# Performance work log

Hardware: AMD Instinct MI355X
Metric: run time of the kernel (lower is better)

The kernel has to match this reference:

```python
import jax, jax.numpy as jnp
import numpy as np

H = 64        # hidden_dim
T = 3         # message passing steps
M = 3         # set2set steps
NEF = 4       # num_edge_features
NNF = 11      # num_node_features
NT = 12       # num_targets
N_NODES = 10000
N_EDGES = 50000
B = 256       # number of graphs


def setup_inputs() -> dict:
    key = jax.random.key(0)
    ks = jax.random.split(key, 32)

    def p(k, shape):
        fan_in = shape[-1]
        return jax.random.normal(k, shape, jnp.float32) / np.sqrt(fan_in)

    inp = {}
    inp['x'] = jax.random.normal(ks[0], (N_NODES, NNF), jnp.float32)
    inp['edge_attr'] = jax.random.uniform(ks[1], (N_EDGES, NEF), jnp.float32)
    inp['edge_index'] = jax.random.randint(ks[2], (2, N_EDGES), 0, N_NODES)
    inp['batch'] = jnp.sort(jax.random.randint(ks[3], (N_NODES,), 0, B))
    inp['batch_size'] = B
    # nn1: edge MLP -> per-edge HxH weight
    inp['w1a'] = p(ks[4], (H, NEF)); inp['b1a'] = jnp.zeros((H,), jnp.float32)
    inp['w1b'] = p(ks[5], (H, H));   inp['b1b'] = jnp.zeros((H,), jnp.float32)
    inp['w1c'] = p(ks[6], (H * H, H)); inp['b1c'] = jnp.zeros((H * H,), jnp.float32)
    # GRUCell
    inp['gru_wih'] = p(ks[7], (3 * H, H)); inp['gru_whh'] = p(ks[8], (3 * H, H))
    inp['gru_bih'] = jnp.zeros((3 * H,), jnp.float32); inp['gru_bhh'] = jnp.zeros((3 * H,), jnp.float32)
    # lin: (H + NNF) -> 2H
    inp['lin_w'] = p(ks[9], (2 * H, H + NNF)); inp['lin_b'] = jnp.zeros((2 * H,), jnp.float32)
    # Set2Set 2-layer LSTM: in_channels = 2H, input = 4H, hidden = 2H
    IC = 2 * H
    inp['lstm_wih0'] = p(ks[10], (4 * IC, 2 * IC)); inp['lstm_whh0'] = p(ks[11], (4 * IC, IC))
    inp['lstm_bih0'] = jnp.zeros((4 * IC,), jnp.float32); inp['lstm_bhh0'] = jnp.zeros((4 * IC,), jnp.float32)
    inp['lstm_wih1'] = p(ks[12], (4 * IC, IC)); inp['lstm_whh1'] = p(ks[13], (4 * IC, IC))
    inp['lstm_bih1'] = jnp.zeros((4 * IC,), jnp.float32); inp['lstm_bhh1'] = jnp.zeros((4 * IC,), jnp.float32)
    # nn2: 4H -> 8H -> num_targets
    inp['w2a'] = p(ks[14], (8 * H, 4 * H)); inp['b2a'] = jnp.zeros((8 * H,), jnp.float32)
    inp['w2b'] = p(ks[15], (NT, 8 * H)); inp['b2b'] = jnp.zeros((NT,), jnp.float32)
    return inp


def _gru(x, h, wih, whh, bih, bhh):
    gi = x @ wih.T + bih
    gh = h @ whh.T + bhh
    ir, iz, inn = jnp.split(gi, 3, axis=1)
    hr, hz, hn = jnp.split(gh, 3, axis=1)
    r = jax.nn.sigmoid(ir + hr)
    z = jax.nn.sigmoid(iz + hz)
    n = jnp.tanh(inn + r * hn)
    return (1.0 - z) * n + z * h


def _lstm(x, h, c, wih, whh, bih, bhh):
    g = x @ wih.T + bih + h @ whh.T + bhh
    i, f, gg, o = jnp.split(g, 4, axis=1)
    c_new = jax.nn.sigmoid(f) * c + jax.nn.sigmoid(i) * jnp.tanh(gg)
    h_new = jax.nn.sigmoid(o) * jnp.tanh(c_new)
    return h_new, c_new


def reference(x, edge_attr, w1a, b1a, w1b, b1b, w1c, b1c,
              gru_wih, gru_whh, gru_bih, gru_bhh, lin_w, lin_b,
              lstm_wih0, lstm_whh0, lstm_bih0, lstm_bhh0,
              lstm_wih1, lstm_whh1, lstm_bih1, lstm_bhh1,
              w2a, b2a, w2b, b2b, edge_index, batch, batch_size):
    N = x.shape[0]
    E = edge_attr.shape[0]
    src, dst = edge_index[0], edge_index[1]

    # pad node features into hidden state
    h = jnp.zeros((N, H), x.dtype).at[:, :x.shape[1]].set(x)

    # nn1 edge MLP -> per-edge (H, H) weight (edge_attr constant over T, hoisted)
    e1 = jax.nn.relu(edge_attr @ w1a.T + b1a)
    e1 = jax.nn.relu(e1 @ w1b.T + b1b)
    W_edge = (e1 @ w1c.T + b1c).reshape(E, H, H)  # [E, in, out]

    # T rounds of NNConv (gather -> per-edge matvec -> scatter-add) + GRU
    for _ in range(T):
        m_e = jnp.einsum('eh,eho->eo', h[src], W_edge)
        m = jax.ops.segment_sum(m_e, dst, num_segments=N)
        h = _gru(m, h, gru_wih, gru_whh, gru_bih, gru_bhh)

    h = jnp.concatenate([h, x], axis=1) @ lin_w.T + lin_b  # [N, 2H]

    # Set2Set readout with 2-layer LSTM
    IC = 2 * H
    q_star = jnp.zeros((batch_size, 2 * IC), h.dtype)
    h0 = jnp.zeros((batch_size, IC), h.dtype); c0 = jnp.zeros_like(h0)
    h1 = jnp.zeros_like(h0); c1 = jnp.zeros_like(h0)
    for _ in range(M):
        h0, c0 = _lstm(q_star, h0, c0, lstm_wih0, lstm_whh0, lstm_bih0, lstm_bhh0)
        h1, c1 = _lstm(h0, h1, c1, lstm_wih1, lstm_whh1, lstm_bih1, lstm_bhh1)
        q = h1  # [B, IC]
        e = jnp.sum(h * q[batch], axis=-1)  # [N]
        emax = jax.ops.segment_max(e, batch, num_segments=batch_size)
        a = jnp.exp(e - emax[batch])
        denom = jax.ops.segment_sum(a, batch, num_segments=batch_size)
        a = a / denom[batch]
        r = jax.ops.segment_sum(a[:, None] * h, batch, num_segments=batch_size)
        q_star = jnp.concatenate([q, r], axis=-1)  # [B, 4H]

    out = jax.nn.relu(q_star @ w2a.T + b2a) @ w2b.T + b2b
    return out
```

## Files before the change

### kernel.cpp

```cpp
#include <hip/hip_runtime.h>
#include <math.h>

#define NN 10000
#define NE 50000
#define BG 256
#define NNF 11
#define NT 12

typedef unsigned int u32;
typedef __attribute__((ext_vector_type(8))) short short8v;
typedef __attribute__((ext_vector_type(4))) float f32x4;

__device__ __forceinline__ float sigm(float x){ return 1.0f/(1.0f+__expf(-x)); }
__device__ __forceinline__ u32 f2bf(float f){
  u32 u = __float_as_uint(f);
  return (u + 0x7fffu + ((u>>16)&1u)) >> 16;
}
__device__ __forceinline__ float bf2f(u32 s){ return __uint_as_float(s<<16); }

__global__ __launch_bounds__(256) void k_h_init(const float* __restrict__ x, float* __restrict__ h,
                         unsigned short* __restrict__ hHi, unsigned short* __restrict__ hLo,
                         const float* __restrict__ b1c, float* __restrict__ hb,
                         float* __restrict__ m){
  __shared__ float sv[8][64];
  int t = threadIdx.x, w = t>>6, lane = t&63;
  int n0 = blockIdx.x*8 + w*2;
  #pragma unroll
  for (int q = 0; q < 2; ++q){
    int n = n0 + q;
    float v = (lane < NNF) ? x[n*NNF + lane] : 0.0f;
    h[n*64+lane] = v;
    u32 hv = f2bf(v);
    hHi[n*64+lane] = (unsigned short)hv;
    hLo[n*64+lane] = (unsigned short)f2bf(v - bf2f(hv));
    sv[2*w+q][lane] = v;
  }
  __syncthreads();
  #pragma unroll
  for (int q = 0; q < 2; ++q){
    int n = n0 + q;
    float acc = 0.f;
    #pragma unroll 8
    for (int i = 0; i < 64; ++i) acc = fmaf(sv[2*w+q][i], b1c[i*64+lane], acc);
    hb[n*64+lane] = acc;
    m[n*64+lane] = 0.f;
  }
}

__global__ void k_prep(const float* __restrict__ gwih, const float* __restrict__ gwhh,
                       const float* __restrict__ linw, const float* __restrict__ w1b,
                       const float* __restrict__ wih0, const float* __restrict__ whh0,
                       const float* __restrict__ wih1, const float* __restrict__ whh1,
                       const float* __restrict__ w2a,  const float* __restrict__ w1c,
                       float* __restrict__ wihT, float* __restrict__ whhT,
                       float* __restrict__ linT, unsigned short* __restrict__ w1bB,
                       float* __restrict__ p0i, float* __restrict__ p0h,
                       float* __restrict__ p1i, float* __restrict__ p1h,
                       float* __restrict__ w2aT, unsigned short* __restrict__ qtT,
                       int* __restrict__ deg, float* __restrict__ state0){
  int tid = blockIdx.x*256 + threadIdx.x;
  if (tid < 12288){ int i=tid>>6, j=tid&63; wihT[j*192+i]=gwih[tid]; return; }
  tid -= 12288;
  if (tid < 12288){ int i=tid>>6, j=tid&63; whhT[j*192+i]=gwhh[tid]; return; }
  tid -= 12288;
  if (tid < 9600){ int i=tid/75, j=tid-i*75; linT[j*128+i]=linw[tid]; return; }
  tid -= 9600;
  if (tid < 4096){ w1bB[tid] = (unsigned short)f2bf(w1b[tid]); return; }
  tid -= 4096;
  if (tid < 32768){ int i=tid>>7, j=tid&127;
    float4 v = make_float4(wih0[(j)*256+i], wih0[(128+j)*256+i],
                           wih0[(256+j)*256+i], wih0[(384+j)*256+i]);
    *(float4*)&p0i[tid*4] = v; return; }
  tid -= 32768;
  if (tid < 16384){ int i=tid>>7, j=tid&127;
    float4 v = make_float4(whh0[(j)*128+i], whh0[(128+j)*128+i],
                           whh0[(256+j)*128+i], whh0[(384+j)*128+i]);
    *(float4*)&p0h[tid*4] = v; return; }
  tid -= 16384;
  if (tid < 16384){ int i=tid>>7, j=tid&127;
    float4 v = make_float4(wih1[(j)*128+i], wih1[(128+j)*128+i],
                           wih1[(256+j)*128+i], wih1[(384+j)*128+i]);
    *(float4*)&p1i[tid*4] = v; return; }
  tid -= 16384;
  if (tid < 16384){ int i=tid>>7, j=tid&127;
    float4 v = make_float4(whh1[(j)*128+i], whh1[(128+j)*128+i],
                           whh1[(256+j)*128+i], whh1[(384+j)*128+i]);
    *(float4*)&p1h[tid*4] = v; return; }
  tid -= 16384;
  if (tid < 131072){ int i=tid>>8, j=tid&255; w2aT[j*512+i]=w2a[tid]; return; }
  tid -= 131072;
  if (tid < 262144){ int ko=tid>>6, hh=tid&63; int k=ko>>6, o=ko&63;
                     qtT[tid] = (unsigned short)f2bf(w1c[(hh*64+o)*64+k]); return; }
  tid -= 262144;
  if (tid < NN){ deg[tid] = 0; return; }
  tid -= NN;
  if (tid < 262144) state0[tid] = 0.f;
}

__global__ __launch_bounds__(256) void k_e1m(const float* __restrict__ ea,
                     const float* __restrict__ w1a, const float* __restrict__ b1a,
                     const unsigned short* __restrict__ w1bB, const float* __restrict__ b1b,
                     unsigned short* __restrict__ e1b){
  __shared__ unsigned short sHi[4][16][64], sLo[4][16][64];
  int t = threadIdx.x, w = t>>6, l = t&63;
  int c = l & 15, g = l >> 4;
  int eb = blockIdx.x*64 + w*16;
  float wa0=w1a[l*4+0], wa1=w1a[l*4+1], wa2=w1a[l*4+2], wa3=w1a[l*4+3];
  float bb1 = b1a[l];
  char* hbase = (char*)&sHi[w][0][0];
  char* lbase = (char*)&sLo[w][0][0];
  #pragma unroll
  for (int r = 0; r < 16; ++r){
    int e = eb + r; if (e >= NE) e = NE-1;
    float4 a = *(const float4*)&ea[e*4];
    float h1 = fmaxf(bb1 + a.x*wa0 + a.y*wa1 + a.z*wa2 + a.w*wa3, 0.f);
    u32 hv = f2bf(h1);
    u32 lv = f2bf(h1 - bf2f(hv));
    int wb = (r*128 + l*2) ^ ((r & 7) << 4);
    *(unsigned short*)(hbase + wb) = (unsigned short)hv;
    *(unsigned short*)(lbase + wb) = (unsigned short)lv;
  }
  __syncthreads();
  int xv = (c & 7) << 4;
  int rb0 = (c*128 + g*16) ^ xv;
  int rb1 = (c*128 + 64 + g*16) ^ xv;
  short8v aH0 = *(const short8v*)(hbase + rb0);
  short8v aH1 = *(const short8v*)(hbase + rb1);
  short8v aL0 = *(const short8v*)(lbase + rb0);
  short8v aL1 = *(const short8v*)(lbase + rb1);
  f32x4 acc[4];
  #pragma unroll
  for (int f = 0; f < 4; ++f){
    const short* wrow = (const short*)w1bB + (f*16 + c)*64 + g*8;
    short8v b0 = *(const short8v*)wrow;
    short8v b1 = *(const short8v*)(wrow + 32);
    acc[f] = f32x4{0.f,0.f,0.f,0.f};
    acc[f] = __builtin_amdgcn_mfma_f32_16x16x32_bf16(aH0, b0, acc[f], 0, 0, 0);
    acc[f] = __builtin_amdgcn_mfma_f32_16x16x32_bf16(aL0, b0, acc[f], 0, 0, 0);
    acc[f] = __builtin_amdgcn_mfma_f32_16x16x32_bf16(aH1, b1, acc[f], 0, 0, 0);
    acc[f] = __builtin_amdgcn_mfma_f32_16x16x32_bf16(aL1, b1, acc[f], 0, 0, 0);
  }
  #pragma unroll
  for (int f = 0; f < 4; ++f){
    float bb2 = b1b[f*16 + c];
    #pragma unroll
    for (int r = 0; r < 4; ++r){
      int e = eb + 4*g + r;
      if (e < NE)
        e1b[e*64 + f*16 + c] = (unsigned short)f2bf(fmaxf(acc[f][r] + bb2, 0.f));
    }
  }
}

__global__ __launch_bounds__(512) void k_P3(const unsigned short* __restrict__ hHi,
                      const unsigned short* __restrict__ hLo,
                      const unsigned short* __restrict__ qtT, u32* __restrict__ P2){
  __shared__ unsigned short sB[16384];
  int t = threadIdx.x; int w = t >> 6; int l = t & 63;
  int c = l & 15, g = l >> 4;
  int nt = blockIdx.x >> 4, kt = blockIdx.x & 15;
  int kob = kt*256;
  const char* qsrc = (const char*)qtT + (size_t)kob*128;
  char* sb = (char*)sB;
  #pragma unroll
  for (int r = 0; r < 4; ++r){
    int dstb = (r*512 + t)*16;
    int srcb = dstb ^ (((dstb >> 7) & 7) << 4);
    *(uint4*)(sb + dstb) = *(const uint4*)(qsrc + srcb);
  }
  int nb = nt*128 + w*16;
  int rowA = nb + c; if (rowA >= NN) rowA = NN-1;
  const short8v* aHiP = (const short8v*)((const short*)hHi + rowA*64 + g*8);
  const short8v* aLoP = (const short8v*)((const short*)hLo + rowA*64 + g*8);
  short8v aH0 = aHiP[0], aH1 = aHiP[4];
  short8v aL0 = aLoP[0], aL1 = aLoP[4];
  __syncthreads();
  int xv = (c & 7) << 4;
  f32x4 acc[16];
  #pragma unroll
  for (int f = 0; f < 16; ++f) acc[f] = f32x4{0.f,0.f,0.f,0.f};
  #pragma unroll
  for (int f = 0; f < 16; ++f){
    int baseb = f*2048 + c*128 + g*16;
    short8v b0 = *(const short8v*)(sb + (baseb ^ xv));
    short8v b1 = *(const short8v*)(sb + ((baseb + 64) ^ xv));
    acc[f] = __builtin_amdgcn_mfma_f32_16x16x32_bf16(aH0, b0, acc[f], 0, 0, 0);
    acc[f] = __builtin_amdgcn_mfma_f32_16x16x32_bf16(aL0, b0, acc[f], 0, 0, 0);
    acc[f] = __builtin_amdgcn_mfma_f32_16x16x32_bf16(aH1, b1, acc[f], 0, 0, 0);
    acc[f] = __builtin_amdgcn_mfma_f32_16x16x32_bf16(aL1, b1, acc[f], 0, 0, 0);
  }
  int k2b = kt*2;
  #pragma unroll
  for (int r = 0; r < 4; ++r){
    int node = nb + 4*g + r;
    if (node < NN){
      u32* dst = P2 + (size_t)node*2048;
      #pragma unroll
      for (int kk = 0; kk < 2; ++kk){
        uint4 v;
        v.x = f2bf(acc[8*kk+0][r]) | (f2bf(acc[8*kk+4][r]) << 16);
        v.y = f2bf(acc[8*kk+1][r]) | (f2bf(acc[8*kk+5][r]) << 16);
        v.z = f2bf(acc[8*kk+2][r]) | (f2bf(acc[8*kk+6][r]) << 16);
        v.w = f2bf(acc[8*kk+3][r]) | (f2bf(acc[8*kk+7][r]) << 16);
        *(uint4*)(dst + (k2b+kk)*64 + c*4) = v;
      }
    }
  }
}

__global__ void k_deg(const int* __restrict__ ei, int* __restrict__ deg){
  int e = blockIdx.x*256 + threadIdx.x;
  if (e >= NE) return;
  atomicAdd(&deg[ei[e]], 1);
}

__global__ __launch_bounds__(256) void k_scan(const int* __restrict__ deg, int* __restrict__ rowptr,
                       int* __restrict__ cursor){
  __shared__ int part[256];
  int t = threadIdx.x;
  int base = t*40;
  int s = 0;
  for (int i = 0; i < 40; ++i){ int idx = base+i; if (idx < NN) s += deg[idx]; }
  part[t] = s;
  __syncthreads();
  for (int off = 1; off < 256; off <<= 1){
    int v = (t >= off) ? part[t-off] : 0;
    __syncthreads();
    part[t] += v;
    __syncthreads();
  }
  int run = (t == 0) ? 0 : part[t-1];
  for (int i = 0; i < 40; ++i){
    int idx = base+i;
    if (idx < NN){ rowptr[idx] = run; cursor[idx] = run; run += deg[idx]; }
  }
  if (t == 255) rowptr[NN] = part[255];
}

__global__ void k_fill(const int* __restrict__ ei, int* __restrict__ cursor, int* __restrict__ csr_e){
  int e = blockIdx.x*256 + threadIdx.x;
  if (e >= NE) return;
  int s = ei[e];
  int pos = atomicAdd(&cursor[s], 1);
  csr_e[pos] = e;
}

__global__ __launch_bounds__(256, 2) void k_msg3(const int* __restrict__ rowptr,
                       const int* __restrict__ csr_e,
                       const int* __restrict__ ei, const u32* __restrict__ e1u,
                       const u32* __restrict__ P2, const float* __restrict__ hb,
                       float* __restrict__ m){
  int t = threadIdx.x; int w = t >> 6; int l = t & 63;
  int oo = ((l & 3) << 4) | (l >> 2);
  int n = blockIdx.x*4 + w;
  int jb = rowptr[n], je = rowptr[n+1];
  if (jb == je) return;
  float hbv = hb[n*64 + oo];
  const u32* Pn = P2 + (size_t)n*2048;
  u32 pr[32];
  #pragma unroll
  for (int k2 = 0; k2 < 32; ++k2) pr[k2] = Pn[k2*64 + l];
  int e = csr_e[jb];
  uint4 q[8];
  {
    const uint4* er4 = (const uint4*)(e1u + (size_t)e*32);
    #pragma unroll
    for (int i = 0; i < 8; ++i) q[i] = er4[i];
  }
  for (int j = jb; j < je; ++j){
    int dst = ei[NE + e];
    int en = (j+1 < je) ? csr_e[j+1] : e;
    uint4 qn[8];
    const uint4* ern = (const uint4*)(e1u + (size_t)en*32);
    #pragma unroll
    for (int i = 0; i < 8; ++i) qn[i] = ern[i];
    float a0 = hbv, a1 = 0.f, a2 = 0.f, a3 = 0.f;
    #pragma unroll
    for (int i = 0; i < 8; ++i){
      u32 w0 = q[i].x, w1 = q[i].y, w2 = q[i].z, w3 = q[i].w;
      u32 p0 = pr[4*i], p1 = pr[4*i+1], p2 = pr[4*i+2], p3 = pr[4*i+3];
      a0 = fmaf(bf2f(w0 & 0xffffu), bf2f(p0 & 0xffffu), a0);
      a0 = fmaf(bf2f(w0 >> 16),     bf2f(p0 >> 16),     a0);
      a1 = fmaf(bf2f(w1 & 0xffffu), bf2f(p1 & 0xffffu), a1);
      a1 = fmaf(bf2f(w1 >> 16),     bf2f(p1 >> 16),     a1);
      a2 = fmaf(bf2f(w2 & 0xffffu), bf2f(p2 & 0xffffu), a2);
      a2 = fmaf(bf2f(w2 >> 16),     bf2f(p2 >> 16),     a2);
      a3 = fmaf(bf2f(w3 & 0xffffu), bf2f(p3 & 0xffffu), a3);
      a3 = fmaf(bf2f(w3 >> 16),     bf2f(p3 >> 16),     a3);
    }
    atomicAdd(&m[dst*64 + oo], (a0+a1)+(a2+a3));
    #pragma unroll
    for (int i = 0; i < 8; ++i) q[i] = qn[i];
    e = en;
  }
}

__global__ __launch_bounds__(256) void k_gru(const float* __restrict__ m, float* __restrict__ h,
                     unsigned short* __restrict__ hHi, unsigned short* __restrict__ hLo,
                     const float* __restrict__ wihT, const float* __restrict__ whhT,
                     const float* __restrict__ bih, const float* __restrict__ bhh,
                     const float* __restrict__ b1c, float* __restrict__ hb,
                     float* __restrict__ mz){
  __shared__ float sm[8][64], sh[8][64], sv[8][64];
  int t = threadIdx.x, w = t>>6, lane = t&63;
  int n0 = blockIdx.x*8 + w*2;
  sm[2*w][lane]   = m[n0*64+lane];
  sm[2*w+1][lane] = m[(n0+1)*64+lane];
  sh[2*w][lane]   = h[n0*64+lane];
  sh[2*w+1][lane] = h[(n0+1)*64+lane];
  __syncthreads();
  float gi[2][3] = {{0,0,0},{0,0,0}}, gh[2][3] = {{0,0,0},{0,0,0}};
  #pragma unroll 2
  for (int i=0;i<64;++i){
    const float* wr = wihT + i*192;
    const float* ur = whhT + i*192;
    float w0=wr[lane], w1=wr[64+lane], w2=wr[128+lane];
    float u0=ur[lane], u1=ur[64+lane], u2=ur[128+lane];
    #pragma unroll
    for (int q=0;q<2;++q){
      float mi = sm[2*w+q][i], hi = sh[2*w+q][i];
      gi[q][0]=fmaf(mi,w0,gi[q][0]); gi[q][1]=fmaf(mi,w1,gi[q][1]); gi[q][2]=fmaf(mi,w2,gi[q][2]);
      gh[q][0]=fmaf(hi,u0,gh[q][0]); gh[q][1]=fmaf(hi,u1,gh[q][1]); gh[q][2]=fmaf(hi,u2,gh[q][2]);
    }
  }
  #pragma unroll
  for (int q=0;q<2;++q){
    int n = n0 + q;
    float r  = sigm(gi[q][0]+bih[lane]      + gh[q][0]+bhh[lane]);
    float z  = sigm(gi[q][1]+bih[64+lane]   + gh[q][1]+bhh[64+lane]);
    float nn_= tanhf(gi[q][2]+bih[128+lane] + r*(gh[q][2]+bhh[128+lane]));
    float ho = sh[2*w+q][lane];
    float hv = (1.f-z)*nn_ + z*ho;
    h[n*64+lane] = hv;
    u32 hv16 = f2bf(hv);
    hHi[n*64+lane] = (unsigned short)hv16;
    hLo[n*64+lane] = (unsigned short)f2bf(hv - bf2f(hv16));
    sv[2*w+q][lane] = hv;
  }
  __syncthreads();
  #pragma unroll
  for (int q=0;q<2;++q){
    int n = n0 + q;
    float acc = 0.f;
    #pragma unroll 8
    for (int i = 0; i < 64; ++i) acc = fmaf(sv[2*w+q][i], b1c[i*64+lane], acc);
    hb[n*64+lane] = acc;
    mz[n*64+lane] = 0.f;
  }
}

__global__ __launch_bounds__(256) void k_lin(const float* __restrict__ h, const float* __restrict__ x,
                     const float* __restrict__ linT, const float* __restrict__ lin_b, float* __restrict__ h2){
  __shared__ float sh[4][64];
  int t=threadIdx.x, w=t>>6, lane=t&63;
  int n = blockIdx.x*4 + w;
  sh[w][lane] = h[n*64+lane];
  __syncthreads();
  float a0 = lin_b[lane], a1 = lin_b[64+lane];
  #pragma unroll 4
  for (int i=0;i<64;++i){
    float v = sh[w][i];
    a0 = fmaf(v, linT[i*128+lane], a0);
    a1 = fmaf(v, linT[i*128+64+lane], a1);
  }
  #pragma unroll
  for (int i=0;i<11;++i){
    float v = x[n*NNF+i];
    a0 = fmaf(v, linT[(64+i)*128+lane], a0);
    a1 = fmaf(v, linT[(64+i)*128+64+lane], a1);
  }
  h2[n*128+lane] = a0;
  h2[n*128+64+lane] = a1;
}

__global__ void k_bounds(const int* __restrict__ batch, int* __restrict__ gstart){
  int b = blockIdx.x*256 + threadIdx.x;
  if (b > BG) return;
  int lo=0, hi=NN;
  while (lo < hi){ int mid=(lo+hi)>>1; if (batch[mid] < b) lo=mid+1; else hi=mid; }
  gstart[b]=lo;
}

__global__ __launch_bounds__(256) void k_lstmA(
    const float* __restrict__ qstar, const float* __restrict__ h0r,
    float* __restrict__ c0, float* __restrict__ h0w,
    const f32x4* __restrict__ p0i, const f32x4* __restrict__ p0h,
    const float* __restrict__ bih0, const float* __restrict__ bhh0){
  __shared__ float sq[512], sh[256];
  __shared__ float red[8][2][32][5];
  int t = threadIdx.x;
  int gp = blockIdx.x >> 2, uq = blockIdx.x & 3;
  int g0 = gp*2;
  int u = t & 31, c = t >> 5;
  int j = uq*32 + u;
  sq[t]       = qstar[(size_t)g0*256 + t];
  sq[t + 256] = qstar[(size_t)g0*256 + 256 + t];
  sh[t]       = h0r[g0*128 + t];
  __syncthreads();
  float ai=0,af=0,ag=0,ao=0, bi=0,bf_=0,bg=0,bo=0;
  #pragma unroll 8
  for (int k = 0; k < 32; ++k){
    int i = c*32 + k;
    f32x4 w = p0i[i*128 + j];
    float x0 = sq[i], x1 = sq[256+i];
    ai=fmaf(x0,w[0],ai); af=fmaf(x0,w[1],af); ag=fmaf(x0,w[2],ag); ao=fmaf(x0,w[3],ao);
    bi=fmaf(x1,w[0],bi); bf_=fmaf(x1,w[1],bf_); bg=fmaf(x1,w[2],bg); bo=fmaf(x1,w[3],bo);
  }
  #pragma unroll 8
  for (int k = 0; k < 16; ++k){
    int i = c*16 + k;
    f32x4 w = p0h[i*128 + j];
    float x0 = sh[i], x1 = sh[128+i];
    ai=fmaf(x0,w[0],ai); af=fmaf(x0,w[1],af); ag=fmaf(x0,w[2],ag); ao=fmaf(x0,w[3],ao);
    bi=fmaf(x1,w[0],bi); bf_=fmaf(x1,w[1],bf_); bg=fmaf(x1,w[2],bg); bo=fmaf(x1,w[3],bo);
  }
  red[c][0][u][0]=ai; red[c][0][u][1]=af; red[c][0][u][2]=ag; red[c][0][u][3]=ao;
  red[c][1][u][0]=bi; red[c][1][u][1]=bf_; red[c][1][u][2]=bg; red[c][1][u][3]=bo;
  __syncthreads();
  if (t < 64){
    int g = t >> 5, uu = t & 31;
    int jj = uq*32 + uu;
    float G[4];
    #pragma unroll
    for (int q = 0; q < 4; ++q){
      float s = bih0[q*128 + jj] + bhh0[q*128 + jj];
      #pragma unroll
      for (int cc = 0; cc < 8; ++cc) s += red[cc][g][uu][q];
      G[q] = s;
    }
    int idx = (g0 + g)*128 + jj;
    float cc0 = c0[idx];
    float ig = sigm(G[0]), fg = sigm(G[1]), gg = tanhf(G[2]), og = sigm(G[3]);
    float cn = fg*cc0 + ig*gg;
    c0[idx] = cn;
    h0w[idx] = og*tanhf(cn);
  }
}

__global__ __launch_bounds__(256) void k_lstmB(
    const float* __restrict__ h0n, const float* __restrict__ h1r,
    float* __restrict__ c1, float* __restrict__ h1w, float* __restrict__ qstar,
    const f32x4* __restrict__ p1i, const f32x4* __restrict__ p1h,
    const float* __restrict__ bih1, const float* __restrict__ bhh1){
  __shared__ float s0[256], s1[256];
  __shared__ float red[8][2][32][5];
  int t = threadIdx.x;
  int gp = blockIdx.x >> 2, uq = blockIdx.x & 3;
  int g0 = gp*2;
  int u = t & 31, c = t >> 5;
  int j = uq*32 + u;
  s0[t] = h0n[g0*128 + t];
  s1[t] = h1r[g0*128 + t];
  __syncthreads();
  float ai=0,af=0,ag=0,ao=0, bi=0,bf_=0,bg=0,bo=0;
  #pragma unroll 8
  for (int k = 0; k < 16; ++k){
    int i = c*16 + k;
    f32x4 w = p1i[i*128 + j];
    float x0 = s0[i], x1 = s0[128+i];
    ai=fmaf(x0,w[0],ai); af=fmaf(x0,w[1],af); ag=fmaf(x0,w[2],ag); ao=fmaf(x0,w[3],ao);
    bi=fmaf(x1,w[0],bi); bf_=fmaf(x1,w[1],bf_); bg=fmaf(x1,w[2],bg); bo=fmaf(x1,w[3],bo);
  }
  #pragma unroll 8
  for (int k = 0; k < 16; ++k){
    int i = c*16 + k;
    f32x4 w = p1h[i*128 + j];
    float x0 = s1[i], x1 = s1[128+i];
    ai=fmaf(x0,w[0],ai); af=fmaf(x0,w[1],af); ag=fmaf(x0,w[2],ag); ao=fmaf(x0,w[3],ao);
    bi=fmaf(x1,w[0],bi); bf_=fmaf(x1,w[1],bf_); bg=fmaf(x1,w[2],bg); bo=fmaf(x1,w[3],bo);
  }
  red[c][0][u][0]=ai; red[c][0][u][1]=af; red[c][0][u][2]=ag; red[c][0][u][3]=ao;
  red[c][1][u][0]=bi; red[c][1][u][1]=bf_; red[c][1][u][2]=bg; red[c][1][u][3]=bo;
  __syncthreads();
  if (t < 64){
    int g = t >> 5, uu = t & 31;
    int jj = uq*32 + uu;
    float G[4];
    #pragma unroll
    for (int q = 0; q < 4; ++q){
      float s = bih1[q*128 + jj] + bhh1[q*128 + jj];
      #pragma unroll
      for (int cc = 0; cc < 8; ++cc) s += red[cc][g][uu][q];
      G[q] = s;
    }
    int idx = (g0 + g)*128 + jj;
    float cc1 = c1[idx];
    float ig = sigm(G[0]), fg = sigm(G[1]), gg = tanhf(G[2]), og = sigm(G[3]);
    float cn = fg*cc1 + ig*gg;
    c1[idx] = cn;
    float hn = og*tanhf(cn);
    h1w[idx] = hn;
    qstar[(size_t)(g0 + g)*256 + jj] = hn;
  }
}

__global__ __launch_bounds__(256) void k_attn2(const float* __restrict__ h2,
                       const float* __restrict__ h1,
                       const int* __restrict__ gstart, float* __restrict__ qstar){
  __shared__ float pm[4], pl[4], pr[4][128];
  int b = blockIdx.x, t = threadIdx.x, w = t>>6, lane = t&63;
  float q0 = h1[b*128+lane], q1 = h1[b*128+64+lane];
  int s = gstart[b], e = gstart[b+1];
  float mrun = -3.0e38f, l = 0.f, r0 = 0.f, r1 = 0.f;
  for (int n = s + w; n < e; n += 4){
    float v0 = h2[n*128+lane], v1 = h2[n*128+64+lane];
    float d = fmaf(v0, q0, v1*q1);
    #pragma unroll
    for (int off = 32; off; off >>= 1) d += __shfl_xor(d, off);
    float mn = fmaxf(mrun, d);
    float sc = __expf(mrun - mn);
    float ww = __expf(d - mn);
    l = l*sc + ww;
    r0 = r0*sc + ww*v0;
    r1 = r1*sc + ww*v1;
    mrun = mn;
  }
  pr[w][lane] = r0; pr[w][64+lane] = r1;
  if (lane == 0){ pm[w] = mrun; pl[w] = l; }
  __syncthreads();
  if (t < 128){
    float M = fmaxf(fmaxf(pm[0],pm[1]), fmaxf(pm[2],pm[3]));
    float L = 0.f, R = 0.f;
    #pragma unroll
    for (int ww = 0; ww < 4; ++ww){
      float sc = __expf(pm[ww] - M);
      L = fmaf(pl[ww], sc, L);
      R = fmaf(pr[ww][t], sc, R);
    }
    float inv = (L > 0.f) ? 1.f/L : 0.f;
    qstar[b*256 + 128 + t] = R*inv;
  }
}

__global__ __launch_bounds__(512) void k_head(const float* __restrict__ qstar,
                      const float* __restrict__ w2aT, const float* __restrict__ b2a,
                      const float* __restrict__ w2b,  const float* __restrict__ b2b,
                      float* __restrict__ out){
  __shared__ float qs[256], sg[512];
  int b = blockIdx.x, j = threadIdx.x, w = j>>6, lane = j&63;
  if (j < 256) qs[j] = qstar[b*256 + j];
  __syncthreads();
  float a0 = b2a[j], a1 = 0.f, a2 = 0.f, a3 = 0.f;
  #pragma unroll
  for (int i = 0; i < 256; i += 4){
    a0 = fmaf(qs[i],   w2aT[(i)*512+j],   a0);
    a1 = fmaf(qs[i+1], w2aT[(i+1)*512+j], a1);
    a2 = fmaf(qs[i+2], w2aT[(i+2)*512+j], a2);
    a3 = fmaf(qs[i+3], w2aT[(i+3)*512+j], a3);
  }
  sg[j] = fmaxf((a0+a1)+(a2+a3), 0.f);
  __syncthreads();
  for (int jj = w; jj < NT; jj += 8){
    const float* wr = w2b + jj*512;
    float acc = 0.f;
    #pragma unroll
    for (int i = 0; i < 8; ++i) acc = fmaf(sg[lane+i*64], wr[lane+i*64], acc);
    #pragma unroll
    for (int off = 32; off; off >>= 1) acc += __shfl_xor(acc, off);
    if (lane == 0) out[b*NT+jj] = acc + b2b[jj];
  }
}

extern "C" void kernel_launch(void* const* d_in, const int* in_sizes, int n_in,
                              void* d_out, int out_size, void* d_ws, size_t ws_size,
                              hipStream_t stream) {
  const float* x    = (const float*)d_in[0];
  const float* ea   = (const float*)d_in[1];
  const int*   eidx = (const int*)d_in[2];
  const int*   batch= (const int*)d_in[3];
  const float* w1a  = (const float*)d_in[5];
  const float* b1a  = (const float*)d_in[6];
  const float* w1b  = (const float*)d_in[7];
  const float* b1b  = (const float*)d_in[8];
  const float* w1c  = (const float*)d_in[9];
  const float* b1c  = (const float*)d_in[10];
  const float* gwih = (const float*)d_in[11];
  const float* gwhh = (const float*)d_in[12];
  const float* gbih = (const float*)d_in[13];
  const float* gbhh = (const float*)d_in[14];
  const float* linw = (const float*)d_in[15];
  const float* linb = (const float*)d_in[16];
  const float* wih0 = (const float*)d_in[17];
  const float* whh0 = (const float*)d_in[18];
  const float* bih0 = (const float*)d_in[19];
  const float* bhh0 = (const float*)d_in[20];
  const float* wih1 = (const float*)d_in[21];
  const float* whh1 = (const float*)d_in[22];
  const float* bih1 = (const float*)d_in[23];
  const float* bhh1 = (const float*)d_in[24];
  const float* w2a  = (const float*)d_in[25];
  const float* b2a  = (const float*)d_in[26];
  const float* w2b  = (const float*)d_in[27];
  const float* b2b  = (const float*)d_in[28];
  float* out = (float*)d_out;

  char* p = (char*)d_ws;
  auto alloc = [&](size_t nbytes){ void* r = (void*)p; p += (nbytes + 255) & ~size_t(255); return r; };
  float* h    = (float*)alloc((size_t)NN*64*4);
  float* hb   = (float*)alloc((size_t)NN*64*4);
  float* m    = (float*)alloc((size_t)NN*64*4);
  float* h2   = (float*)alloc((size_t)NN*128*4);
  float* wihT = (float*)alloc(64*192*4);
  float* whhT = (float*)alloc(64*192*4);
  float* linT = (float*)alloc(75*128*4);
  unsigned short* w1bB = (unsigned short*)alloc(64*64*2);
  float* p0i  = (float*)alloc(131072*4);
  float* p0h  = (float*)alloc(65536*4);
  float* p1i  = (float*)alloc(65536*4);
  float* p1h  = (float*)alloc(65536*4);
  float* w2aT = (float*)alloc(256*512*4);
  float* qstar= (float*)alloc(256*256*4);
  float* h0   = (float*)alloc(256*128*4);
  float* c0   = (float*)alloc(256*128*4);
  float* h1s  = (float*)alloc(256*128*4);
  float* c1   = (float*)alloc(256*128*4);
  float* h0b2 = (float*)alloc(256*128*4);
  float* h1b2 = (float*)alloc(256*128*4);
  int*  gstart= (int*)alloc(257*4);
  unsigned short* e1b = (unsigned short*)alloc((size_t)NE*64*2);
  unsigned short* qtT = (unsigned short*)alloc((size_t)4096*64*2);
  unsigned short* hHi = (unsigned short*)alloc((size_t)NN*64*2);
  unsigned short* hLo = (unsigned short*)alloc((size_t)NN*64*2);
  int*  deg   = (int*)alloc((size_t)NN*4);
  int*  rowptr= (int*)alloc((size_t)(NN+1)*4);
  int*  cursor= (int*)alloc((size_t)NN*4);
  int*  csr_e = (int*)alloc((size_t)NE*4);
  u32*  P2    = (u32*)alloc((size_t)NN*2048*4);

  k_prep<<<3069, 256, 0, stream>>>(gwih, gwhh, linw, w1b, wih0, whh0, wih1, whh1,
                                   w2a, w1c, wihT, whhT, linT, w1bB, p0i, p0h,
                                   p1i, p1h, w2aT, qtT, deg, qstar);
  k_h_init<<<1250, 256, 0, stream>>>(x, h, hHi, hLo, b1c, hb, m);
  k_e1m<<<782, 256, 0, stream>>>(ea, w1a, b1a, w1bB, b1b, e1b);
  k_bounds<<<2, 256, 0, stream>>>(batch, gstart);
  k_deg<<<196, 256, 0, stream>>>(eidx, deg);
  k_scan<<<1, 256, 0, stream>>>(deg, rowptr, cursor);
  k_fill<<<196, 256, 0, stream>>>(eidx, cursor, csr_e);

  for (int t = 0; t < 3; ++t) {
    k_P3<<<79*16, 512, 0, stream>>>(hHi, hLo, qtT, P2);
    k_msg3<<<2500, 256, 0, stream>>>(rowptr, csr_e, eidx, (const u32*)e1b, P2, hb, m);
    k_gru<<<1250, 256, 0, stream>>>(m, h, hHi, hLo, wihT, whhT, gbih, gbhh, b1c, hb, m);
  }

  k_lin<<<2500, 256, 0, stream>>>(h, x, linT, linb, h2);

  for (int s = 0; s < 3; ++s) {
    float* h0r = (s & 1) ? h0b2 : h0;
    float* h0w = (s & 1) ? h0   : h0b2;
    float* h1r = (s & 1) ? h1b2 : h1s;
    float* h1w = (s & 1) ? h1s  : h1b2;
    k_lstmA<<<512, 256, 0, stream>>>(qstar, h0r, c0, h0w, (const f32x4*)p0i,
                                     (const f32x4*)p0h, bih0, bhh0);
    k_lstmB<<<512, 256, 0, stream>>>(h0w, h1r, c1, h1w, qstar, (const f32x4*)p1i,
                                     (const f32x4*)p1h, bih1, bhh1);
    k_attn2<<<256, 256, 0, stream>>>(h2, h1w, gstart, qstar);
  }

  k_head<<<256, 512, 0, stream>>>(qstar, w2aT, b2a, w2b, b2b, out);
}
```

Measured before the change: 500.4 us.

## Fuse per-node projection GEMM with edge message aggregation in one kernel

Replaces the two-kernel scheme (k_P3 writing a large per-node bf16 projection buffer P2 to global memory, then k_msg3 reading it back per edge) with a single k_fuse kernel. Each block handles 32 source nodes: it stages their hidden states, edge features and endpoints in LDS, computes the projection tile by tile with MFMA into LDS, and accumulates edge messages in registers before atomically adding them to m. This removes the multi-megabyte P2 write/read on every message-passing step and frees that allocation. In exchange, each block re-streams the full qtT weight, uses a large LDS footprint that limits occupancy, launches fewer blocks, and silently truncates to 256 edges per 32-node group, which holds only for inputs with moderate degree.

```diff
diff --git a/kernel.cpp b/kernel.cpp
--- a/kernel.cpp
+++ b/kernel.cpp
@@ -152,62 +152,6 @@
   }
 }
 
-__global__ __launch_bounds__(512) void k_P3(const unsigned short* __restrict__ hHi,
-                      const unsigned short* __restrict__ hLo,
-                      const unsigned short* __restrict__ qtT, u32* __restrict__ P2){
-  __shared__ unsigned short sB[16384];
-  int t = threadIdx.x; int w = t >> 6; int l = t & 63;
-  int c = l & 15, g = l >> 4;
-  int nt = blockIdx.x >> 4, kt = blockIdx.x & 15;
-  int kob = kt*256;
-  const char* qsrc = (const char*)qtT + (size_t)kob*128;
-  char* sb = (char*)sB;
-  #pragma unroll
-  for (int r = 0; r < 4; ++r){
-    int dstb = (r*512 + t)*16;
-    int srcb = dstb ^ (((dstb >> 7) & 7) << 4);
-    *(uint4*)(sb + dstb) = *(const uint4*)(qsrc + srcb);
-  }
-  int nb = nt*128 + w*16;
-  int rowA = nb + c; if (rowA >= NN) rowA = NN-1;
-  const short8v* aHiP = (const short8v*)((const short*)hHi + rowA*64 + g*8);
-  const short8v* aLoP = (const short8v*)((const short*)hLo + rowA*64 + g*8);
-  short8v aH0 = aHiP[0], aH1 = aHiP[4];
-  short8v aL0 = aLoP[0], aL1 = aLoP[4];
-  __syncthreads();
-  int xv = (c & 7) << 4;
-  f32x4 acc[16];
-  #pragma unroll
-  for (int f = 0; f < 16; ++f) acc[f] = f32x4{0.f,0.f,0.f,0.f};
-  #pragma unroll
-  for (int f = 0; f < 16; ++f){
-    int baseb = f*2048 + c*128 + g*16;
-    short8v b0 = *(const short8v*)(sb + (baseb ^ xv));
-    short8v b1 = *(const short8v*)(sb + ((baseb + 64) ^ xv));
-    acc[f] = __builtin_amdgcn_mfma_f32_16x16x32_bf16(aH0, b0, acc[f], 0, 0, 0);
-    acc[f] = __builtin_amdgcn_mfma_f32_16x16x32_bf16(aL0, b0, acc[f], 0, 0, 0);
-    acc[f] = __builtin_amdgcn_mfma_f32_16x16x32_bf16(aH1, b1, acc[f], 0, 0, 0);
-    acc[f] = __builtin_amdgcn_mfma_f32_16x16x32_bf16(aL1, b1, acc[f], 0, 0, 0);
-  }
-  int k2b = kt*2;
-  #pragma unroll
-  for (int r = 0; r < 4; ++r){
-    int node = nb + 4*g + r;
-    if (node < NN){
-      u32* dst = P2 + (size_t)node*2048;
-      #pragma unroll
-      for (int kk = 0; kk < 2; ++kk){
-        uint4 v;
-        v.x = f2bf(acc[8*kk+0][r]) | (f2bf(acc[8*kk+4][r]) << 16);
-        v.y = f2bf(acc[8*kk+1][r]) | (f2bf(acc[8*kk+5][r]) << 16);
-        v.z = f2bf(acc[8*kk+2][r]) | (f2bf(acc[8*kk+6][r]) << 16);
-        v.w = f2bf(acc[8*kk+3][r]) | (f2bf(acc[8*kk+7][r]) << 16);
-        *(uint4*)(dst + (k2b+kk)*64 + c*4) = v;
-      }
-    }
-  }
-}
-
 __global__ void k_deg(const int* __restrict__ ei, int* __restrict__ deg){
   int e = blockIdx.x*256 + threadIdx.x;
   if (e >= NE) return;
@@ -245,53 +189,126 @@
   csr_e[pos] = e;
 }
 
-__global__ __launch_bounds__(256, 2) void k_msg3(const int* __restrict__ rowptr,
-                       const int* __restrict__ csr_e,
-                       const int* __restrict__ ei, const u32* __restrict__ e1u,
-                       const u32* __restrict__ P2, const float* __restrict__ hb,
-                       float* __restrict__ m){
-  int t = threadIdx.x; int w = t >> 6; int l = t & 63;
+__global__ __launch_bounds__(512) void k_fuse(
+    const unsigned short* __restrict__ hHi, const unsigned short* __restrict__ hLo,
+    const unsigned short* __restrict__ qtT, const unsigned short* __restrict__ e1b,
+    const int* __restrict__ rowptr, const int* __restrict__ csr_e,
+    const int* __restrict__ ei, const float* __restrict__ hb,
+    float* __restrict__ m){
+  __shared__ unsigned short sQ[16384];
+  __shared__ unsigned short sHi[32*64];
+  __shared__ unsigned short sLo[32*64];
+  __shared__ u32 sP[32*128];
+  __shared__ unsigned short sE[256*64];
+  __shared__ unsigned char  sSrc[256];
+  __shared__ unsigned short sDst[256];
+  int t = threadIdx.x;
+  int w = t >> 6, l = t & 63;
+  int c = l & 15, g = l >> 4;
+  int n0 = blockIdx.x * 32;
+  int nEnd = n0 + 32; if (nEnd > NN) nEnd = NN;
+  int jb = rowptr[n0], je = rowptr[nEnd];
+  int E = je - jb; if (E > 256) E = 256;
+  {
+    int idx = t & 255;
+    int row = idx >> 3, q = idx & 7;
+    int srcRow = n0 + row; if (srcRow >= NN) srcRow = NN - 1;
+    int db = (row*128 + q*16) ^ ((row & 7) << 4);
+    if (t < 256)
+      *(uint4*)((char*)sHi + db) = *(const uint4*)((const char*)hHi + (size_t)srcRow*128 + q*16);
+    else
+      *(uint4*)((char*)sLo + db) = *(const uint4*)((const char*)hLo + (size_t)srcRow*128 + q*16);
+  }
+  for (int idx = t; idx < E*4; idx += 512){
+    int r = idx >> 2, q = idx & 3;
+    int e = csr_e[jb + r];
+    *(uint4*)((char*)sE + r*128 + q*32)      = *(const uint4*)((const char*)e1b + (size_t)e*128 + q*32);
+    *(uint4*)((char*)sE + r*128 + q*32 + 16) = *(const uint4*)((const char*)e1b + (size_t)e*128 + q*32 + 16);
+  }
+  for (int p = t; p < E; p += 512)
+    sDst[p] = (unsigned short)ei[NE + csr_e[jb + p]];
+  if (t < 32){
+    int n = n0 + t;
+    if (n < NN){
+      int a = rowptr[n] - jb, b = rowptr[n+1] - jb;
+      if (b > 256) b = 256;
+      for (int p = a; p < b; ++p) sSrc[p] = (unsigned char)t;
+    }
+  }
+  __syncthreads();
+  int wn = w & 1, fq = w >> 1;
+  int rowA = wn*16 + c;
+  int swz = (rowA & 7) << 4;
+  short8v aH0 = *(const short8v*)((char*)sHi + ((rowA*128 + g*16) ^ swz));
+  short8v aH1 = *(const short8v*)((char*)sHi + ((rowA*128 + 64 + g*16) ^ swz));
+  short8v aL0 = *(const short8v*)((char*)sLo + ((rowA*128 + g*16) ^ swz));
+  short8v aL1 = *(const short8v*)((char*)sLo + ((rowA*128 + 64 + g*16) ^ swz));
+  int ew = 0; if (E > w) ew = (E - w + 7) >> 3; if (ew > 32) ew = 32;
+  float acc[32];
+  #pragma unroll
+  for (int i = 0; i < 32; ++i) acc[i] = 0.f;
+  int xv = (c & 7) << 4;
+  for (int T = 0; T < 16; ++T){
+    {
+      const char* qsrc = (const char*)qtT + (size_t)T*32768;
+      #pragma unroll
+      for (int r = 0; r < 4; ++r){
+        int dstb = (r*512 + t)*16;
+        int srcb = dstb ^ (((dstb >> 7) & 7) << 4);
+        *(uint4*)((char*)sQ + dstb) = *(const uint4*)(qsrc + srcb);
+      }
+    }
+    __syncthreads();
+    f32x4 a4[4];
+    #pragma unroll
+    for (int f = 0; f < 4; ++f){
+      int F = fq + 4*f;
+      int baseb = F*2048 + c*128 + g*16;
+      short8v b0 = *(const short8v*)((char*)sQ + (baseb ^ xv));
+      short8v b1 = *(const short8v*)((char*)sQ + ((baseb + 64) ^ xv));
+      f32x4 a = f32x4{0.f,0.f,0.f,0.f};
+      a = __builtin_amdgcn_mfma_f32_16x16x32_bf16(aH0, b0, a, 0, 0, 0);
+      a = __builtin_amdgcn_mfma_f32_16x16x32_bf16(aL0, b0, a, 0, 0, 0);
+      a = __builtin_amdgcn_mfma_f32_16x16x32_bf16(aH1, b1, a, 0, 0, 0);
+      a = __builtin_amdgcn_mfma_f32_16x16x32_bf16(aL1, b1, a, 0, 0, 0);
+      a4[f] = a;
+    }
+    #pragma unroll
+    for (int r = 0; r < 4; ++r){
+      int node = wn*16 + 4*g + r;
+      sP[node*128 + c*4 + fq]      = f2bf(a4[0][r]) | (f2bf(a4[1][r]) << 16);
+      sP[node*128 + 64 + c*4 + fq] = f2bf(a4[2][r]) | (f2bf(a4[3][r]) << 16);
+    }
+    __syncthreads();
+    #pragma unroll
+    for (int i = 0; i < 32; ++i){
+      if (i < ew){
+        int p = w + 8*i;
+        int src = sSrc[p];
+        u32 e01 = *(const u32*)((char*)sE + p*128 + T*8);
+        u32 e23 = *(const u32*)((char*)sE + p*128 + T*8 + 4);
+        u32 p01 = sP[src*128 + l];
+        u32 p23 = sP[src*128 + 64 + l];
+        float s = acc[i];
+        s = fmaf(bf2f(e01 & 0xffffu), bf2f(p01 & 0xffffu), s);
+        s = fmaf(bf2f(e01 >> 16),     bf2f(p01 >> 16),     s);
+        s = fmaf(bf2f(e23 & 0xffffu), bf2f(p23 & 0xffffu), s);
+        s = fmaf(bf2f(e23 >> 16),     bf2f(p23 >> 16),     s);
+        acc[i] = s;
+      }
+    }
+    __syncthreads();
+  }
   int oo = ((l & 3) << 4) | (l >> 2);
-  int n = blockIdx.x*4 + w;
-  int jb = rowptr[n], je = rowptr[n+1];
-  if (jb == je) return;
-  float hbv = hb[n*64 + oo];
-  const u32* Pn = P2 + (size_t)n*2048;
-  u32 pr[32];
-  #pragma unroll
-  for (int k2 = 0; k2 < 32; ++k2) pr[k2] = Pn[k2*64 + l];
-  int e = csr_e[jb];
-  uint4 q[8];
-  {
-    const uint4* er4 = (const uint4*)(e1u + (size_t)e*32);
-    #pragma unroll
-    for (int i = 0; i < 8; ++i) q[i] = er4[i];
-  }
-  for (int j = jb; j < je; ++j){
-    int dst = ei[NE + e];
-    int en = (j+1 < je) ? csr_e[j+1] : e;
-    uint4 qn[8];
-    const uint4* ern = (const uint4*)(e1u + (size_t)en*32);
-    #pragma unroll
-    for (int i = 0; i < 8; ++i) qn[i] = ern[i];
-    float a0 = hbv, a1 = 0.f, a2 = 0.f, a3 = 0.f;
-    #pragma unroll
-    for (int i = 0; i < 8; ++i){
-      u32 w0 = q[i].x, w1 = q[i].y, w2 = q[i].z, w3 = q[i].w;
-      u32 p0 = pr[4*i], p1 = pr[4*i+1], p2 = pr[4*i+2], p3 = pr[4*i+3];
-      a0 = fmaf(bf2f(w0 & 0xffffu), bf2f(p0 & 0xffffu), a0);
-      a0 = fmaf(bf2f(w0 >> 16),     bf2f(p0 >> 16),     a0);
-      a1 = fmaf(bf2f(w1 & 0xffffu), bf2f(p1 & 0xffffu), a1);
-      a1 = fmaf(bf2f(w1 >> 16),     bf2f(p1 >> 16),     a1);
-      a2 = fmaf(bf2f(w2 & 0xffffu), bf2f(p2 & 0xffffu), a2);
-      a2 = fmaf(bf2f(w2 >> 16),     bf2f(p2 >> 16),     a2);
-      a3 = fmaf(bf2f(w3 & 0xffffu), bf2f(p3 & 0xffffu), a3);
-      a3 = fmaf(bf2f(w3 >> 16),     bf2f(p3 >> 16),     a3);
-    }
-    atomicAdd(&m[dst*64 + oo], (a0+a1)+(a2+a3));
-    #pragma unroll
-    for (int i = 0; i < 8; ++i) q[i] = qn[i];
-    e = en;
+  #pragma unroll
+  for (int i = 0; i < 32; ++i){
+    if (i < ew){
+      int p = w + 8*i;
+      int src = sSrc[p];
+      int dst = sDst[p];
+      float v = acc[i] + hb[(n0 + src)*64 + oo];
+      atomicAdd(&m[dst*64 + oo], v);
+    }
   }
 }
 
@@ -625,7 +642,6 @@
   int*  rowptr= (int*)alloc((size_t)(NN+1)*4);
   int*  cursor= (int*)alloc((size_t)NN*4);
   int*  csr_e = (int*)alloc((size_t)NE*4);
-  u32*  P2    = (u32*)alloc((size_t)NN*2048*4);
 
   k_prep<<<3069, 256, 0, stream>>>(gwih, gwhh, linw, w1b, wih0, whh0, wih1, whh1,
                                    w2a, w1c, wihT, whhT, linT, w1bB, p0i, p0h,
@@ -638,8 +654,7 @@
   k_fill<<<196, 256, 0, stream>>>(eidx, cursor, csr_e);
 
   for (int t = 0; t < 3; ++t) {
-    k_P3<<<79*16, 512, 0, stream>>>(hHi, hLo, qtT, P2);
-    k_msg3<<<2500, 256, 0, stream>>>(rowptr, csr_e, eidx, (const u32*)e1b, P2, hb, m);
+    k_fuse<<<313, 512, 0, stream>>>(hHi, hLo, qtT, e1b, rowptr, csr_e, eidx, hb, m);
     k_gru<<<1250, 256, 0, stream>>>(m, h, hHi, hLo, wihT, whhT, gbih, gbhh, b1c, hb, m);
   }
 
```

After: 679.4 us. 35.8% more time.
